# Kernel optimization log

Measured on AMD Instinct MI355X. Metric: run time of the kernel, lower is better.

The kernel has to match this reference:

```python
import jax, jax.numpy as jnp
import numpy as np

IN_DIM = 256
QK_DIM = IN_DIM // 8


def setup_inputs() -> dict:
    key = jax.random.key(0)
    ks = jax.random.split(key, 10)
    B, C, W, H = 4, IN_DIM, 64, 64
    a = jax.random.normal(ks[0], (B, C, W, H), dtype=jnp.float32)
    b = jax.random.normal(ks[1], (B, C, W, H), dtype=jnp.float32)
    c = jax.random.uniform(ks[2], (B, 1, 2 * W, 2 * H), dtype=jnp.float32)
    scale = 0.02
    wq = jax.random.normal(ks[3], (QK_DIM, C), dtype=jnp.float32) * scale
    bq = jnp.zeros((QK_DIM,), dtype=jnp.float32)
    wk = jax.random.normal(ks[4], (QK_DIM, C), dtype=jnp.float32) * scale
    bk = jnp.zeros((QK_DIM,), dtype=jnp.float32)
    wv = jax.random.normal(ks[5], (C, C), dtype=jnp.float32) * scale
    bv = jnp.zeros((C,), dtype=jnp.float32)
    gamma = jnp.ones((1,), dtype=jnp.float32)
    return {"a": a, "b": b, "c": c, "wq": wq, "bq": bq, "wk": wk,
            "bk": bk, "wv": wv, "bv": bv, "gamma": gamma}


def reference(a, b, c, wq, bq, wk, bk, wv, bv, gamma):
    B, C, W, H = a.shape
    N = W * H
    # F.interpolate(c, scale_factor=1/down_rate, mode='nearest'): output idx i -> input idx i*down_rate
    down = c.shape[2] // W
    cd = c[:, :, ::down, ::down]                      # [B,1,W,H]
    # 1x1 convs as channel contractions
    q = jnp.einsum('bchw,oc->bohw', a, wq) + bq[None, :, None, None]
    k = jnp.einsum('bchw,oc->bohw', b, wk) + bk[None, :, None, None]
    v = jnp.einsum('bchw,oc->bohw', a, wv) + bv[None, :, None, None]
    qf = q.reshape(B, QK_DIM, N)                      # proj_query^T rows are spatial
    kf = k.reshape(B, QK_DIM, N)
    vf = v.reshape(B, C, N)
    sim = jnp.einsum('bdi,bdj->bij', qf, kf)          # [B,N,N]
    cflat = cd.reshape(B, N)
    # mask[b,i,j] = cflat[b,i] (per-query multiplicative logit scaling)
    logits = sim * cflat[:, :, None]
    attn = jax.nn.softmax(logits, axis=-1)            # [B,N,N]
    out_attn = jnp.einsum('bcj,bij->bci', vf, attn).reshape(B, C, W, H)
    out = gamma * a * cd + (1.0 - cd) * out_attn
    return out
```

## Files before the change

### kernel.cpp

```cpp
#include <hip/hip_runtime.h>

#define LOG2E 1.44269504088896340736f

typedef __attribute__((ext_vector_type(8))) short short8;
typedef __attribute__((ext_vector_type(4))) float float4v;
typedef __attribute__((ext_vector_type(2))) float float2v;
typedef __attribute__((ext_vector_type(2))) int int2v;
typedef __attribute__((ext_vector_type(4))) int int4v;

__device__ inline unsigned short f2bf(float f) {
    union { float f; unsigned u; } v; v.f = f;
    unsigned r = v.u + 0x7fffu + ((v.u >> 16) & 1u);
    return (unsigned short)(r >> 16);
}
__device__ inline float bf2f(unsigned short u) {
    union { unsigned u; float f; } v; v.u = ((unsigned)u) << 16;
    return v.f;
}
__device__ inline unsigned pk_bf16(float a, float b) {
    union { float f; unsigned u; } ua, ub; ua.f = a; ub.f = b;
    return __builtin_amdgcn_perm(ub.u + 0x8000u, ua.u + 0x8000u, 0x07060302u);
}
__device__ inline unsigned cvtpk_bf16(float a, float b) {
    unsigned r;
    asm("v_cvt_pk_bf16_f32 %0, %1, %2" : "=v"(r) : "v"(a), "v"(b));
    return r;
}

__global__ void wcvt_kernel(const float* __restrict__ wq, const float* __restrict__ wk,
                            const float* __restrict__ wv, unsigned short* __restrict__ Wbf)
{
    int idx = blockIdx.x * 256 + threadIdx.x;
    int e4  = idx * 4;
    int row = e4 >> 8, col = e4 & 255;
    const float* src = (row < 32) ? (wq + row * 256 + col)
                     : (row < 64) ? (wk + (row - 32) * 256 + col)
                                  : (wv + (row - 64) * 256 + col);
    float4v v = *(const float4v*)src;
    int2v p;
    p.x = (unsigned)f2bf(v[0]) | ((unsigned)f2bf(v[1]) << 16);
    p.y = (unsigned)f2bf(v[2]) | ((unsigned)f2bf(v[3]) << 16);
    *(int2v*)(Wbf + e4) = p;
}

__launch_bounds__(512, 2)
__global__ void proj_kernel(const float* __restrict__ a_p, const float* __restrict__ b_p,
                            const float* __restrict__ c_p,
                            const float* __restrict__ bq, const float* __restrict__ bk,
                            const float* __restrict__ bv,
                            const unsigned short* __restrict__ Wbf,
                            unsigned short* __restrict__ Qg, unsigned short* __restrict__ Kg,
                            unsigned short* __restrict__ Vg)
{
    __shared__ __align__(16) unsigned short At[64 * 266];
    __shared__ __align__(16) unsigned short Bt[64 * 266];
    __shared__ float bias[320];
    __shared__ float cdl[64];

    const int t    = threadIdx.x;
    const int blk  = blockIdx.x;
    const int b    = blk & 3;
    const int tile = blk >> 2;
    const int i0   = tile * 64;
    const int lane = t & 63;
    const int w    = t >> 6;
    const int q    = lane >> 4;
    const int n    = lane & 15;
    const int it   = w & 3;
    const int mh   = w >> 2;

    {
        const int arr = t >> 8, tt = t & 255;
        unsigned* dst = (unsigned*)(arr ? Bt : At);
        const float* base = (arr ? b_p : a_p) + (size_t)b * 256 * 4096 + i0;
#pragma unroll
        for (int r = 0; r < 8; ++r) {
            int task = r * 256 + tt;
            int cp = task >> 4, px4 = (task & 15) * 4;
            const float* s0 = base + (size_t)(2 * cp) * 4096 + px4;
            float4v r0 = *(const float4v*)s0;
            float4v r1 = *(const float4v*)(s0 + 4096);
#pragma unroll
            for (int k = 0; k < 4; ++k)
                dst[(px4 + k) * 133 + cp] = pk_bf16(r0[k], r1[k]);
        }
        if (t < 320) bias[t] = (t < 32) ? bq[t] : (t < 64) ? bk[t - 32] : bv[t - 64];
        else if (t < 384) cdl[t - 320] = c_p[b * 16384 + tile * 256 + (t - 320) * 2];
    }
    __syncthreads();

    float4v acc[10];
#pragma unroll
    for (int j = 0; j < 10; ++j) acc[j] = (float4v){0.f, 0.f, 0.f, 0.f};

#pragma unroll 2
    for (int kc = 0; kc < 8; ++kc) {
        short8 xa = *(const short8*)&At[(it * 16 + n) * 266 + kc * 32 + q * 8];
        short8 xb = xa;
        if (mh == 0)
            xb = *(const short8*)&Bt[(it * 16 + n) * 266 + kc * 32 + q * 8];
#pragma unroll
        for (int j = 0; j < 10; ++j) {
            int mt = mh * 10 + j;
            short8 wf = *(const short8*)(Wbf + (size_t)(mt * 16 + n) * 256 + kc * 32 + q * 8);
            short8 bsel = (mt == 2 || mt == 3) ? xb : xa;
            acc[j] = __builtin_amdgcn_mfma_f32_16x16x32_bf16(wf, bsel, acc[j], 0, 0, 0);
        }
    }
    __syncthreads();

    unsigned short* QKst = At;
    unsigned short* Vst  = Bt;
    {
        const float cdq = cdl[it * 16 + n] * LOG2E;
#pragma unroll
        for (int j = 0; j < 10; ++j) {
            int mt = mh * 10 + j;
            float4v bv4 = *(const float4v*)&bias[mt * 16 + q * 4];
            float v0 = acc[j][0] + bv4[0], v1 = acc[j][1] + bv4[1];
            float v2 = acc[j][2] + bv4[2], v3 = acc[j][3] + bv4[3];
            if (mt < 2) {
                v0 *= cdq; v1 *= cdq; v2 *= cdq; v3 *= cdq;
                int2v pk; pk.x = (int)pk_bf16(v0, v1); pk.y = (int)pk_bf16(v2, v3);
                *(int2v*)&QKst[(it * 16 + n) * 72 + mt * 16 + q * 4] = pk;
            } else if (mt < 4) {
                int2v pk; pk.x = (int)pk_bf16(v0, v1); pk.y = (int)pk_bf16(v2, v3);
                *(int2v*)&QKst[(it * 16 + n) * 72 + mt * 16 + q * 4] = pk;
            } else {
                int p = ((n >> 2) * 8) + ((it & 1) * 4) + (n & 3);
                int cbase = mt * 16 - 64 + q * 4;
                int jb = it >> 1;
                Vst[((jb * 256) + cbase + 0) * 32 + p] = f2bf(v0);
                Vst[((jb * 256) + cbase + 1) * 32 + p] = f2bf(v1);
                Vst[((jb * 256) + cbase + 2) * 32 + p] = f2bf(v2);
                Vst[((jb * 256) + cbase + 3) * 32 + p] = f2bf(v3);
            }
        }
    }
    __syncthreads();

    {
        int i = t >> 3, h8 = t & 7;
        int4v v = *(const int4v*)&QKst[i * 72 + h8 * 8];
        unsigned short* dstp = (h8 < 4)
            ? Qg + (size_t)(b * 4096 + i0 + i) * 32 + h8 * 8
            : Kg + (size_t)(b * 4096 + i0 + i) * 32 + (h8 - 4) * 8;
        *(int4v*)dstp = v;
    }
    {
#pragma unroll
        for (int k = 0; k < 4; ++k) {
            int flat = k * 512 + t;
            int4v v = *(const int4v*)&Vst[flat * 8];
            int jb = flat >> 10;
            *(int4v*)(Vg + (size_t)(b * 128 + tile * 2 + jb) * 8192 + (flat & 1023) * 8) = v;
        }
    }
}

__launch_bounds__(256, 3)
__global__ void attn_kernel(const unsigned short* __restrict__ Qg,
                            const unsigned short* __restrict__ Kg,
                            const unsigned short* __restrict__ Vg,
                            unsigned short* __restrict__ Opart, float* __restrict__ lsum)
{
    const int t    = threadIdx.x;
    const int blk  = blockIdx.x;
    const int b    = blk & 3;
    const int s_lo = (blk >> 2) & 1;
    const int rt   = (blk >> 3) & 63;
    const int s    = s_lo + 2 * (blk >> 9);
    const int lidx = (s << 8) | (rt << 2) | b;
    const int i0   = rt * 64;
    const int lane = t & 63;
    const int w    = t >> 6;
    const int q    = lane >> 4;
    const int n    = lane & 15;

    short8 qf[4];
#pragma unroll
    for (int ig = 0; ig < 4; ++ig)
        qf[ig] = *(const short8*)(Qg + (size_t)(b * 4096 + i0 + ig * 16 + n) * 32 + q * 8);

    float4v acc[4][4];
#pragma unroll
    for (int ig = 0; ig < 4; ++ig)
#pragma unroll
        for (int ct = 0; ct < 4; ++ct) acc[ig][ct] = (float4v){0.f, 0.f, 0.f, 0.f};
    float lsc[4] = {0.f, 0.f, 0.f, 0.f};

    const float4v m16v = (float4v){-16.f, -16.f, -16.f, -16.f};

    const unsigned short* kb = Kg + (size_t)(b * 4096 + s * 1024 + n) * 32 + q * 8;
    const unsigned short* vb = Vg + ((size_t)((b * 128 + s * 32) * 256 + w * 64 + n)) * 32 + q * 8;

    short8 vf[4];
#pragma unroll
    for (int ct = 0; ct < 4; ++ct)
        vf[ct] = *(const short8*)(vb + ct * 512);
    short8 kf0 = *(const short8*)(kb);
    short8 kf1 = *(const short8*)(kb + 512);

    short8 pfc[4];
    {
        float4v s0[4], s1[4];
#pragma unroll
        for (int ig = 0; ig < 4; ++ig) {
            s0[ig] = __builtin_amdgcn_mfma_f32_16x16x32_bf16(kf0, qf[ig], m16v, 0, 0, 0);
            s1[ig] = __builtin_amdgcn_mfma_f32_16x16x32_bf16(kf1, qf[ig], m16v, 0, 0, 0);
        }
        kf0 = *(const short8*)(kb + 1024);
        kf1 = *(const short8*)(kb + 1536);
#pragma unroll
        for (int ig = 0; ig < 4; ++ig) {
            float p0 = __builtin_amdgcn_exp2f(s0[ig][0]), p1 = __builtin_amdgcn_exp2f(s0[ig][1]);
            float p2 = __builtin_amdgcn_exp2f(s0[ig][2]), p3 = __builtin_amdgcn_exp2f(s0[ig][3]);
            float p4 = __builtin_amdgcn_exp2f(s1[ig][0]), p5 = __builtin_amdgcn_exp2f(s1[ig][1]);
            float p6 = __builtin_amdgcn_exp2f(s1[ig][2]), p7 = __builtin_amdgcn_exp2f(s1[ig][3]);
            lsc[ig] += ((p0 + p1) + (p2 + p3)) + ((p4 + p5) + (p6 + p7));
            union { short8 s8; unsigned u[4]; } pf_;
            pf_.u[0] = cvtpk_bf16(p0, p1);
            pf_.u[1] = cvtpk_bf16(p2, p3);
            pf_.u[2] = cvtpk_bf16(p4, p5);
            pf_.u[3] = cvtpk_bf16(p6, p7);
            pfc[ig] = pf_.s8;
        }
    }
    kb += 2048;
    vb += 8192;

#pragma unroll 1
    for (int it = 0; it < 31; ++it) {
        float4v s0[4], s1[4];
#pragma unroll
        for (int ig = 0; ig < 4; ++ig) {
            s0[ig] = __builtin_amdgcn_mfma_f32_16x16x32_bf16(kf0, qf[ig], m16v, 0, 0, 0);
            s1[ig] = __builtin_amdgcn_mfma_f32_16x16x32_bf16(kf1, qf[ig], m16v, 0, 0, 0);
        }
        kf0 = *(const short8*)(kb);
        kf1 = *(const short8*)(kb + 512);

        __builtin_amdgcn_s_setprio(1);
#pragma unroll
        for (int ig = 0; ig < 4; ++ig)
#pragma unroll
            for (int ct = 0; ct < 4; ++ct)
                acc[ig][ct] = __builtin_amdgcn_mfma_f32_16x16x32_bf16(pfc[ig], vf[ct], acc[ig][ct], 0, 0, 0);
        __builtin_amdgcn_s_setprio(0);

#pragma unroll
        for (int ct = 0; ct < 4; ++ct)
            vf[ct] = *(const short8*)(vb + ct * 512);

#pragma unroll
        for (int ig = 0; ig < 4; ++ig) {
            float p0 = __builtin_amdgcn_exp2f(s0[ig][0]), p1 = __builtin_amdgcn_exp2f(s0[ig][1]);
            float p2 = __builtin_amdgcn_exp2f(s0[ig][2]), p3 = __builtin_amdgcn_exp2f(s0[ig][3]);
            float p4 = __builtin_amdgcn_exp2f(s1[ig][0]), p5 = __builtin_amdgcn_exp2f(s1[ig][1]);
            float p6 = __builtin_amdgcn_exp2f(s1[ig][2]), p7 = __builtin_amdgcn_exp2f(s1[ig][3]);
            lsc[ig] += ((p0 + p1) + (p2 + p3)) + ((p4 + p5) + (p6 + p7));
            union { short8 s8; unsigned u[4]; } pf_;
            pf_.u[0] = cvtpk_bf16(p0, p1);
            pf_.u[1] = cvtpk_bf16(p2, p3);
            pf_.u[2] = cvtpk_bf16(p4, p5);
            pf_.u[3] = cvtpk_bf16(p6, p7);
            pfc[ig] = pf_.s8;
        }

        kb += 1024;
        vb += 8192;
    }

#pragma unroll
    for (int ig = 0; ig < 4; ++ig)
#pragma unroll
        for (int ct = 0; ct < 4; ++ct)
            acc[ig][ct] = __builtin_amdgcn_mfma_f32_16x16x32_bf16(pfc[ig], vf[ct], acc[ig][ct], 0, 0, 0);

    const size_t obase = (size_t)lidx * 16384;
#pragma unroll
    for (int ig = 0; ig < 4; ++ig)
#pragma unroll
        for (int ct = 0; ct < 4; ++ct) {
            int c = w * 64 + ct * 16 + n;
            int i = ig * 16 + q * 4;
            int2v pk;
            pk.x = (int)pk_bf16(acc[ig][ct][0], acc[ig][ct][1]);
            pk.y = (int)pk_bf16(acc[ig][ct][2], acc[ig][ct][3]);
            *(int2v*)(Opart + obase + (size_t)c * 64 + i) = pk;
        }
#pragma unroll
    for (int ig = 0; ig < 4; ++ig) {
        float v = lsc[ig];
        v += __shfl_xor(v, 16, 64);
        v += __shfl_xor(v, 32, 64);
        if (w == 0 && lane < 16)
            lsum[(size_t)lidx * 64 + ig * 16 + lane] = v;
    }
}

__launch_bounds__(256, 4)
__global__ void combine_kernel(const float* __restrict__ a_p, const float* __restrict__ c_p,
                               const float* __restrict__ gamma_p,
                               const unsigned short* __restrict__ Opart,
                               const float* __restrict__ lsum, float* __restrict__ out)
{
    __shared__ float invL[64];
    __shared__ float cdl[64];

    const int t   = threadIdx.x;
    const int blk = blockIdx.x;
    const int b   = blk & 3;
    const int rt  = (blk >> 2) & 63;
    const int cs  = blk >> 8;
    const int i0  = rt * 64;

    if (t < 64) {
        float L = 0.f;
#pragma unroll
        for (int s = 0; s < 4; ++s)
            L += lsum[(size_t)((s << 8) | (rt << 2) | b) * 64 + t];
        invL[t] = 1.0f / L;
        cdl[t] = c_p[b * 16384 + rt * 256 + 2 * t];
    }
    __syncthreads();

    const float gam = gamma_p[0];
    const int il = (t & 31) * 2;
    const int cq = t >> 5;
#pragma unroll
    for (int k = 0; k < 4; ++k) {
        int c = cs * 32 + cq + 8 * k;
        float o0 = 0.f, o1 = 0.f;
#pragma unroll
        for (int s = 0; s < 4; ++s) {
            int idx = (s << 8) | (rt << 2) | b;
            unsigned pr = *(const unsigned*)(Opart + (size_t)idx * 16384 + (size_t)c * 64 + il);
            o0 += bf2f((unsigned short)(pr & 0xffff));
            o1 += bf2f((unsigned short)(pr >> 16));
        }
        o0 *= invL[il];
        o1 *= invL[il + 1];
        size_t gi = (size_t)(b * 256 + c) * 4096 + i0 + il;
        float2v av = *(const float2v*)(a_p + gi);
        float cd0 = cdl[il], cd1 = cdl[il + 1];
        float2v ov;
        ov[0] = gam * av[0] * cd0 + (1.0f - cd0) * o0;
        ov[1] = gam * av[1] * cd1 + (1.0f - cd1) * o1;
        *(float2v*)(out + gi) = ov;
    }
}

extern "C" void kernel_launch(void* const* d_in, const int* in_sizes, int n_in,
                              void* d_out, int out_size, void* d_ws, size_t ws_size,
                              hipStream_t stream)
{
    const float* a_p   = (const float*)d_in[0];
    const float* b_p   = (const float*)d_in[1];
    const float* c_p   = (const float*)d_in[2];
    const float* wq    = (const float*)d_in[3];
    const float* bq    = (const float*)d_in[4];
    const float* wk    = (const float*)d_in[5];
    const float* bk    = (const float*)d_in[6];
    const float* wv    = (const float*)d_in[7];
    const float* bv    = (const float*)d_in[8];
    const float* gamma = (const float*)d_in[9];
    float* out = (float*)d_out;

    unsigned short* Qg    = (unsigned short*)d_ws;
    unsigned short* Kg    = Qg + (size_t)4 * 4096 * 32;
    unsigned short* Vg    = Kg + (size_t)4 * 4096 * 32;
    unsigned short* Wbf   = Vg + (size_t)4 * 256 * 4096;
    unsigned short* Opart = Wbf + (size_t)320 * 256;
    float*          lsum  = (float*)(Opart + (size_t)1024 * 16384);

    wcvt_kernel<<<80, 256, 0, stream>>>(wq, wk, wv, Wbf);
    proj_kernel<<<256, 512, 0, stream>>>(a_p, b_p, c_p, bq, bk, bv, Wbf, Qg, Kg, Vg);
    attn_kernel<<<1024, 256, 0, stream>>>(Qg, Kg, Vg, Opart, lsum);
    combine_kernel<<<2048, 256, 0, stream>>>(a_p, c_p, gamma, Opart, lsum, out);
}
```

Measured before the change: 183.1 us.

## Halve projection tile to 32 pixels and vectorize combine kernel loads

The projection kernel now processes 32 pixels per block instead of 64. This doubles the grid to 512 blocks, halves shared memory use, and raises the occupancy hint to 4 blocks per CU, so more of the 256 CUs stay busy. The wave-to-tile mapping is adjusted to match, with each wave now computing 5 output tiles. The combine kernel now has each thread read 16-byte vectors of partial outputs and handle 8 contiguous pixels, replacing scattered 4-byte loads. The risk is that weight fragments are reloaded by twice as many blocks, and the 32-pixel tile must map correctly onto the 64-row layout of the c mask and V.

```diff
diff --git a/kernel.cpp b/kernel.cpp
--- a/kernel.cpp
+++ b/kernel.cpp
@@ -43,7 +43,7 @@
     *(int2v*)(Wbf + e4) = p;
 }
 
-__launch_bounds__(512, 2)
+__launch_bounds__(512, 4)
 __global__ void proj_kernel(const float* __restrict__ a_p, const float* __restrict__ b_p,
                             const float* __restrict__ c_p,
                             const float* __restrict__ bq, const float* __restrict__ bk,
@@ -52,31 +52,31 @@
                             unsigned short* __restrict__ Qg, unsigned short* __restrict__ Kg,
                             unsigned short* __restrict__ Vg)
 {
-    __shared__ __align__(16) unsigned short At[64 * 266];
-    __shared__ __align__(16) unsigned short Bt[64 * 266];
+    __shared__ __align__(16) unsigned short At[32 * 266];
+    __shared__ __align__(16) unsigned short Bt[32 * 266];
     __shared__ float bias[320];
-    __shared__ float cdl[64];
+    __shared__ float cdl[32];
 
     const int t    = threadIdx.x;
     const int blk  = blockIdx.x;
     const int b    = blk & 3;
     const int tile = blk >> 2;
-    const int i0   = tile * 64;
+    const int i0   = tile * 32;
     const int lane = t & 63;
     const int w    = t >> 6;
     const int q    = lane >> 4;
     const int n    = lane & 15;
-    const int it   = w & 3;
-    const int mh   = w >> 2;
+    const int it   = w & 1;
+    const int mh   = w >> 1;
 
     {
         const int arr = t >> 8, tt = t & 255;
         unsigned* dst = (unsigned*)(arr ? Bt : At);
         const float* base = (arr ? b_p : a_p) + (size_t)b * 256 * 4096 + i0;
 #pragma unroll
-        for (int r = 0; r < 8; ++r) {
+        for (int r = 0; r < 4; ++r) {
             int task = r * 256 + tt;
-            int cp = task >> 4, px4 = (task & 15) * 4;
+            int cp = task >> 3, px4 = (task & 7) * 4;
             const float* s0 = base + (size_t)(2 * cp) * 4096 + px4;
             float4v r0 = *(const float4v*)s0;
             float4v r1 = *(const float4v*)(s0 + 4096);
@@ -85,13 +85,16 @@
                 dst[(px4 + k) * 133 + cp] = pk_bf16(r0[k], r1[k]);
         }
         if (t < 320) bias[t] = (t < 32) ? bq[t] : (t < 64) ? bk[t - 32] : bv[t - 64];
-        else if (t < 384) cdl[t - 320] = c_p[b * 16384 + tile * 256 + (t - 320) * 2];
+        else if (t < 352) {
+            int u = t - 320;
+            cdl[u] = c_p[b * 16384 + (tile >> 1) * 256 + (tile & 1) * 64 + u * 2];
+        }
     }
     __syncthreads();
 
-    float4v acc[10];
-#pragma unroll
-    for (int j = 0; j < 10; ++j) acc[j] = (float4v){0.f, 0.f, 0.f, 0.f};
+    float4v acc[5];
+#pragma unroll
+    for (int j = 0; j < 5; ++j) acc[j] = (float4v){0.f, 0.f, 0.f, 0.f};
 
 #pragma unroll 2
     for (int kc = 0; kc < 8; ++kc) {
@@ -100,8 +103,8 @@
         if (mh == 0)
             xb = *(const short8*)&Bt[(it * 16 + n) * 266 + kc * 32 + q * 8];
 #pragma unroll
-        for (int j = 0; j < 10; ++j) {
-            int mt = mh * 10 + j;
+        for (int j = 0; j < 5; ++j) {
+            int mt = mh * 5 + j;
             short8 wf = *(const short8*)(Wbf + (size_t)(mt * 16 + n) * 256 + kc * 32 + q * 8);
             short8 bsel = (mt == 2 || mt == 3) ? xb : xa;
             acc[j] = __builtin_amdgcn_mfma_f32_16x16x32_bf16(wf, bsel, acc[j], 0, 0, 0);
@@ -114,8 +117,8 @@
     {
         const float cdq = cdl[it * 16 + n] * LOG2E;
 #pragma unroll
-        for (int j = 0; j < 10; ++j) {
-            int mt = mh * 10 + j;
+        for (int j = 0; j < 5; ++j) {
+            int mt = mh * 5 + j;
             float4v bv4 = *(const float4v*)&bias[mt * 16 + q * 4];
             float v0 = acc[j][0] + bv4[0], v1 = acc[j][1] + bv4[1];
             float v2 = acc[j][2] + bv4[2], v3 = acc[j][3] + bv4[3];
@@ -127,19 +130,18 @@
                 int2v pk; pk.x = (int)pk_bf16(v0, v1); pk.y = (int)pk_bf16(v2, v3);
                 *(int2v*)&QKst[(it * 16 + n) * 72 + mt * 16 + q * 4] = pk;
             } else {
-                int p = ((n >> 2) * 8) + ((it & 1) * 4) + (n & 3);
+                int p = ((n >> 2) * 8) + (it * 4) + (n & 3);
                 int cbase = mt * 16 - 64 + q * 4;
-                int jb = it >> 1;
-                Vst[((jb * 256) + cbase + 0) * 32 + p] = f2bf(v0);
-                Vst[((jb * 256) + cbase + 1) * 32 + p] = f2bf(v1);
-                Vst[((jb * 256) + cbase + 2) * 32 + p] = f2bf(v2);
-                Vst[((jb * 256) + cbase + 3) * 32 + p] = f2bf(v3);
+                Vst[(cbase + 0) * 32 + p] = f2bf(v0);
+                Vst[(cbase + 1) * 32 + p] = f2bf(v1);
+                Vst[(cbase + 2) * 32 + p] = f2bf(v2);
+                Vst[(cbase + 3) * 32 + p] = f2bf(v3);
             }
         }
     }
     __syncthreads();
 
-    {
+    if (t < 256) {
         int i = t >> 3, h8 = t & 7;
         int4v v = *(const int4v*)&QKst[i * 72 + h8 * 8];
         unsigned short* dstp = (h8 < 4)
@@ -149,11 +151,10 @@
     }
     {
 #pragma unroll
-        for (int k = 0; k < 4; ++k) {
+        for (int k = 0; k < 2; ++k) {
             int flat = k * 512 + t;
             int4v v = *(const int4v*)&Vst[flat * 8];
-            int jb = flat >> 10;
-            *(int4v*)(Vg + (size_t)(b * 128 + tile * 2 + jb) * 8192 + (flat & 1023) * 8) = v;
+            *(int4v*)(Vg + (size_t)(b * 128 + tile) * 8192 + (size_t)flat * 8) = v;
         }
     }
 }
@@ -326,29 +327,35 @@
     __syncthreads();
 
     const float gam = gamma_p[0];
-    const int il = (t & 31) * 2;
-    const int cq = t >> 5;
-#pragma unroll
-    for (int k = 0; k < 4; ++k) {
-        int c = cs * 32 + cq + 8 * k;
-        float o0 = 0.f, o1 = 0.f;
-#pragma unroll
-        for (int s = 0; s < 4; ++s) {
-            int idx = (s << 8) | (rt << 2) | b;
-            unsigned pr = *(const unsigned*)(Opart + (size_t)idx * 16384 + (size_t)c * 64 + il);
-            o0 += bf2f((unsigned short)(pr & 0xffff));
-            o1 += bf2f((unsigned short)(pr >> 16));
-        }
-        o0 *= invL[il];
-        o1 *= invL[il + 1];
-        size_t gi = (size_t)(b * 256 + c) * 4096 + i0 + il;
-        float2v av = *(const float2v*)(a_p + gi);
-        float cd0 = cdl[il], cd1 = cdl[il + 1];
-        float2v ov;
-        ov[0] = gam * av[0] * cd0 + (1.0f - cd0) * o0;
-        ov[1] = gam * av[1] * cd1 + (1.0f - cd1) * o1;
-        *(float2v*)(out + gi) = ov;
-    }
+    const int c  = cs * 32 + (t >> 3);
+    const int e8 = (t & 7) * 8;
+    float o[8];
+#pragma unroll
+    for (int r = 0; r < 8; ++r) o[r] = 0.f;
+#pragma unroll
+    for (int s = 0; s < 4; ++s) {
+        int idx = (s << 8) | (rt << 2) | b;
+        int4v pv = *(const int4v*)(Opart + (size_t)idx * 16384 + (size_t)c * 64 + e8);
+#pragma unroll
+        for (int h = 0; h < 4; ++h) {
+            unsigned u = (unsigned)pv[h];
+            o[2 * h]     += bf2f((unsigned short)(u & 0xffffu));
+            o[2 * h + 1] += bf2f((unsigned short)(u >> 16));
+        }
+    }
+    size_t gi = (size_t)(b * 256 + c) * 4096 + i0 + e8;
+    float4v a0 = *(const float4v*)(a_p + gi);
+    float4v a1 = *(const float4v*)(a_p + gi + 4);
+    float4v ov0, ov1;
+#pragma unroll
+    for (int r = 0; r < 4; ++r) {
+        float cd0 = cdl[e8 + r],     l0 = invL[e8 + r];
+        float cd1 = cdl[e8 + 4 + r], l1 = invL[e8 + 4 + r];
+        ov0[r] = gam * a0[r] * cd0 + (1.0f - cd0) * (o[r] * l0);
+        ov1[r] = gam * a1[r] * cd1 + (1.0f - cd1) * (o[4 + r] * l1);
+    }
+    *(float4v*)(out + gi) = ov0;
+    *(float4v*)(out + gi + 4) = ov1;
 }
 
 extern "C" void kernel_launch(void* const* d_in, const int* in_sizes, int n_in,
@@ -375,7 +382,7 @@
     float*          lsum  = (float*)(Opart + (size_t)1024 * 16384);
 
     wcvt_kernel<<<80, 256, 0, stream>>>(wq, wk, wv, Wbf);
-    proj_kernel<<<256, 512, 0, stream>>>(a_p, b_p, c_p, bq, bk, bv, Wbf, Qg, Kg, Vg);
+    proj_kernel<<<512, 512, 0, stream>>>(a_p, b_p, c_p, bq, bk, bv, Wbf, Qg, Kg, Vg);
     attn_kernel<<<1024, 256, 0, stream>>>(Qg, Kg, Vg, Opart, lsum);
     combine_kernel<<<2048, 256, 0, stream>>>(a_p, c_p, gamma, Opart, lsum, out);
 }
```

Result: no change. 183.4 us (+0.2%).
